# Performance work log

Measured on AMD Instinct MI355X. Metric: run time of the kernel, lower is better.

Reference implementation:

```python
import jax, jax.numpy as jnp
import numpy as np
import math

EMBED_DIMS = 256
NUM_HEADS = 8
NUM_LEVELS = 4
NUM_POINTS = 8
SPATIAL_SHAPES = np.array([[92, 160], [46, 80], [23, 40], [12, 20]], dtype=np.int32)


def _offset_bias():
    # Faithful to reset_parameters(): per-head unit directions scaled by point index.
    thetas = np.arange(NUM_HEADS, dtype=np.float32) * (2.0 * math.pi / NUM_HEADS)
    grid = np.stack([np.cos(thetas), np.sin(thetas)], axis=-1)
    grid = grid / np.abs(grid).max(axis=-1, keepdims=True)
    grid = np.tile(grid[:, None, None, :], (1, NUM_LEVELS, NUM_POINTS, 1))
    for i in range(NUM_POINTS):
        grid[:, :, i, :] *= i + 1
    return grid.reshape(-1).astype(np.float32)


def setup_inputs() -> dict:
    key = jax.random.key(0)
    ks = jax.random.split(key, 8)
    B, Q, E = 4, 10000, EMBED_DIMS
    S = int((SPATIAL_SHAPES[:, 0] * SPATIAL_SHAPES[:, 1]).sum())
    Z = 4  # num_z_anchors; NUM_POINTS % Z == 0
    query = jax.random.normal(ks[0], (B, Q, E), dtype=jnp.float32)
    value = jax.random.normal(ks[1], (B, S, E), dtype=jnp.float32)
    reference_points = jax.random.uniform(ks[2], (B, Q, Z, 2), dtype=jnp.float32)
    # Learned params (random weights so the math is fully exercised; bias per original init).
    w_off = jax.random.normal(ks[3], (E, NUM_HEADS * NUM_LEVELS * NUM_POINTS * 2), dtype=jnp.float32) * 0.01
    b_off = jnp.asarray(_offset_bias())
    w_attn = jax.random.normal(ks[4], (E, NUM_HEADS * NUM_LEVELS * NUM_POINTS), dtype=jnp.float32) * 0.02
    b_attn = jnp.zeros((NUM_HEADS * NUM_LEVELS * NUM_POINTS,), dtype=jnp.float32)
    w_val = jax.random.normal(ks[5], (E, E), dtype=jnp.float32) * (1.0 / np.sqrt(E))
    b_val = jnp.zeros((E,), dtype=jnp.float32)
    return {
        "query": query, "value": value, "reference_points": reference_points,
        "w_off": w_off, "b_off": b_off, "w_attn": w_attn, "b_attn": b_attn,
        "w_val": w_val, "b_val": b_val,
        "spatial_shapes": jnp.asarray(SPATIAL_SHAPES),
    }


def _bilinear_sample(img, px, py):
    """grid_sample(bilinear, padding=zeros, align_corners=False).
    img: [N, H, W, D]; px, py: [N, Q, P] in pixel coords. Returns [N, Q, P, D]."""
    H, W = img.shape[1], img.shape[2]
    x0 = jnp.floor(px); y0 = jnp.floor(py)
    wx = (px - x0)[..., None]; wy = (py - y0)[..., None]
    x0i = x0.astype(jnp.int32); y0i = y0.astype(jnp.int32)
    x1i = x0i + 1; y1i = y0i + 1
    bidx = jnp.arange(img.shape[0])[:, None, None]
    def gather(yy, xx):
        m = ((yy >= 0) & (yy < H) & (xx >= 0) & (xx < W)).astype(img.dtype)[..., None]
        return img[bidx, jnp.clip(yy, 0, H - 1), jnp.clip(xx, 0, W - 1)] * m
    v00 = gather(y0i, x0i); v01 = gather(y0i, x1i)
    v10 = gather(y1i, x0i); v11 = gather(y1i, x1i)
    return (v00 * (1 - wx) + v01 * wx) * (1 - wy) + (v10 * (1 - wx) + v11 * wx) * wy


def _forward(query, value, reference_points, w_off, b_off, w_attn, b_attn, w_val, b_val, shapes_np):
    B, Q, E = query.shape
    NH, L, NP = NUM_HEADS, shapes_np.shape[0], NUM_POINTS
    D = E // NH
    v = (value @ w_val + b_val).reshape(B, -1, NH, D)  # [B, S, NH, D]
    off = (query @ w_off + b_off).reshape(B, Q, NH, L, NP, 2)
    attn = jax.nn.softmax((query @ w_attn + b_attn).reshape(B, Q, NH, L * NP), axis=-1)
    attn = attn.reshape(B, Q, NH, L, NP)
    # Normalize offsets by (W, H) per level.
    norm = jnp.asarray(np.stack([shapes_np[:, 1], shapes_np[:, 0]], axis=-1), dtype=off.dtype)  # [L,2]
    off = off / norm[None, None, None, :, None, :]
    Z = reference_points.shape[2]
    off = off.reshape(B, Q, NH, L, NP // Z, Z, 2)
    loc = reference_points[:, :, None, None, None, :, :] + off  # [B,Q,NH,L,NP/Z,Z,2]
    loc = loc.reshape(B, Q, NH, L, NP, 2)
    out = jnp.zeros((B, Q, NH, D), dtype=query.dtype)
    start = 0
    for lvl in range(L):
        hl, wl = int(shapes_np[lvl, 0]), int(shapes_np[lvl, 1])
        seg = v[:, start:start + hl * wl]
        start += hl * wl
        img = seg.reshape(B, hl, wl, NH, D).transpose(0, 3, 1, 2, 4).reshape(B * NH, hl, wl, D)
        g = loc[:, :, :, lvl].transpose(0, 2, 1, 3, 4).reshape(B * NH, Q, NP, 2)
        # align_corners=False: pixel = norm_coord * size - 0.5
        px = g[..., 0] * wl - 0.5
        py = g[..., 1] * hl - 0.5
        samp = _bilinear_sample(img, px, py)  # [B*NH, Q, NP, D]
        w = attn[:, :, :, lvl].transpose(0, 2, 1, 3).reshape(B * NH, Q, NP)
        out = out + jnp.einsum('nqpd,nqp->nqd', samp, w).reshape(B, NH, Q, D).transpose(0, 2, 1, 3)
    return out.reshape(B, Q, NH * D)


def reference(query, value, reference_points, w_off, b_off, w_attn, b_attn, w_val, b_val, spatial_shapes):
    shapes_np = np.asarray(spatial_shapes)
    return _forward(query, value, reference_points, w_off, b_off, w_attn, b_attn, w_val, b_val, shapes_np)
```

## Files before the change

kernel.cpp:

```cpp
#include <hip/hip_runtime.h>

#define BATCH    4
#define NQ       10000
#define EMB      256
#define NH       8
#define DH       32
#define NL       4
#define NP       8
#define S_TOTAL  19560
#define NROW     (BATCH * NQ)
#define VROWS    (BATCH * S_TOTAL)

typedef _Float16 half8 __attribute__((ext_vector_type(8)));
typedef _Float16 half4v __attribute__((ext_vector_type(4)));
typedef _Float16 half2v __attribute__((ext_vector_type(2)));
typedef float floatx4 __attribute__((ext_vector_type(4)));

__global__ __launch_bounds__(256) void prep_weights(
    const float* __restrict__ w_off, const float* __restrict__ w_attn,
    const float* __restrict__ w_val, _Float16* __restrict__ wT768,
    _Float16* __restrict__ wvaT) {
  const int tid = blockIdx.x * 256 + threadIdx.x;
  const int n = tid >> 8, k = tid & 255;
  const int c = k >> 3, e = k & 7;
  const int swz = ((c ^ (n & 7)) << 3) + e;
  float v;
  _Float16* dst;
  if (n < 512)      { v = w_off[(size_t)k * 512 + n];          dst = wT768 + (size_t)n * 256; }
  else if (n < 768) { v = w_attn[(size_t)k * 256 + (n - 512)]; dst = wT768 + (size_t)n * 256; }
  else              { v = w_val[(size_t)k * 256 + (n - 768)];  dst = wvaT + (size_t)(n - 768) * 256; }
  dst[swz] = (_Float16)v;
}

template <int NC, int NYS, bool SWZ>
__global__ __launch_bounds__(256, 3) void gemm5(
    const float* __restrict__ A, const _Float16* __restrict__ WTs,
    const float* __restrict__ bias0, const float* __restrict__ bias1,
    int splitc, _Float16* __restrict__ C, int M) {
  __shared__ _Float16 bsm[64 * 256];
  const int t = threadIdx.x;
  const int wave = t >> 6, lane = t & 63;
  const int l15 = lane & 15, quad = lane >> 4;
  const int m0 = blockIdx.x * 128 + wave * 32;
  const int nlo = blockIdx.y * (NC / NYS);
  const int nchunks = (NC / NYS) / 64;

  half8 a[2][8];
  #pragma unroll
  for (int i = 0; i < 2; ++i) {
    const float* Ar = A + (size_t)min(m0 + 16 * i + l15, M - 1) * 256 + quad * 8;
    #pragma unroll
    for (int ks = 0; ks < 8; ++ks) {
      const float4 f0 = *(const float4*)(Ar + ks * 32);
      const float4 f1 = *(const float4*)(Ar + ks * 32 + 4);
      a[i][ks][0] = (_Float16)f0.x; a[i][ks][1] = (_Float16)f0.y;
      a[i][ks][2] = (_Float16)f0.z; a[i][ks][3] = (_Float16)f0.w;
      a[i][ks][4] = (_Float16)f1.x; a[i][ks][5] = (_Float16)f1.y;
      a[i][ks][6] = (_Float16)f1.z; a[i][ks][7] = (_Float16)f1.w;
    }
  }

  const _Float16* src = WTs + (size_t)nlo * 256;

  for (int ch = 0; ch < nchunks; ++ch) {
    __syncthreads();
    #pragma unroll
    for (int i = 0; i < 8; ++i)
      *(half8*)&bsm[t * 8 + i * 2048] = *(const half8*)(src + t * 8 + i * 2048);
    __syncthreads();

    floatx4 acc[2][4] = {};
    #pragma unroll
    for (int ks = 0; ks < 8; ++ks) {
      half8 b[4];
      #pragma unroll
      for (int j = 0; j < 4; ++j)
        b[j] = *(const half8*)&bsm[(16 * j + l15) * 256 +
                                   ((((ks * 4 + quad) ^ (l15 & 7))) << 3)];
      #pragma unroll
      for (int j = 0; j < 4; ++j)
        #pragma unroll
        for (int i = 0; i < 2; ++i)
          acc[i][j] = __builtin_amdgcn_mfma_f32_16x16x32_f16(a[i][ks], b[j], acc[i][j], 0, 0, 0);
    }

    const int nc0 = nlo + ch * 64;
    float bc[4];
    #pragma unroll
    for (int j = 0; j < 4; ++j) {
      const int col = nc0 + 16 * j + l15;
      bc[j] = (col < splitc) ? bias0[col] : bias1[col - splitc];
    }

    #pragma unroll
    for (int i = 0; i < 2; ++i) {
      #pragma unroll
      for (int r = 0; r < 4; ++r) {
        const int row = m0 + 16 * i + quad * 4 + r;
        if (row < M) {
          if (SWZ) {
            const int b = row / S_TOTAL;
            const int s = row - b * S_TOTAL;
            #pragma unroll
            for (int j = 0; j < 4; ++j) {
              const int col = nc0 + 16 * j + l15;
              const size_t dst =
                  (((size_t)b * NH + (col >> 5)) * S_TOTAL + s) * 32 + (col & 31);
              C[dst] = (_Float16)(acc[i][j][r] + bc[j]);
            }
          } else {
            #pragma unroll
            for (int j = 0; j < 4; ++j)
              C[(size_t)row * NC + nc0 + 16 * j + l15] =
                  (_Float16)(acc[i][j][r] + bc[j]);
          }
        }
      }
    }
    src += 64 * 256;
  }
}

__global__ __launch_bounds__(256, 4) void msda_sample(
    const _Float16* __restrict__ vproj,
    const _Float16* __restrict__ fused,
    const float* __restrict__ ref,
    float* __restrict__ out) {
  const int lvl_h[NL] = {92, 46, 23, 12};
  const int lvl_w[NL] = {160, 80, 40, 20};
  const int lvl_s[NL] = {0, 14720, 18400, 19320};

  __shared__ int   addr_s[512];
  __shared__ float wl_s[512];
  __shared__ float wr_s[512];

  const int t   = threadIdx.x;
  const int blk = blockIdx.x;
  const int b   = blk & 3;
  const int q   = blk >> 2;
  const int row = b * NQ + q;

  const int h  = t >> 5;
  const int lp = t & 31;
  const int l  = lp >> 3;
  const int p  = lp & 7;

  const float logit = (float)fused[(size_t)row * 768 + 512 + t];
  float mxv = logit;
  #pragma unroll
  for (int m = 1; m < 32; m <<= 1) mxv = fmaxf(mxv, __shfl_xor(mxv, m));
  const float e = __expf(logit - mxv);
  float sum = e;
  #pragma unroll
  for (int m = 1; m < 32; m <<= 1) sum += __shfl_xor(sum, m);
  const float attnw = e / sum;

  const half2v o2 = *(const half2v*)(fused + (size_t)row * 768 + 2 * t);
  const float ox = (float)o2[0], oy = (float)o2[1];
  const int z = p & 3;
  const float rx = ref[((size_t)row * 4 + z) * 2 + 0];
  const float ry = ref[((size_t)row * 4 + z) * 2 + 1];
  const int Wl = lvl_w[l], Hl = lvl_h[l], st = lvl_s[l];

  const float px = fmaf(rx, (float)Wl, ox) - 0.5f;
  const float py = fmaf(ry, (float)Hl, oy) - 0.5f;
  const float x0f = floorf(px), y0f = floorf(py);
  const float wx = px - x0f, wy = py - y0f;
  const int x0 = (int)x0f, y0 = (int)y0f;
  const int x1 = x0 + 1,   y1 = y0 + 1;

  const float mx0 = (x0 >= 0 && x0 < Wl) ? 1.f : 0.f;
  const float mx1 = (x1 >= 0 && x1 < Wl) ? 1.f : 0.f;
  const float my0 = (y0 >= 0 && y0 < Hl) ? 1.f : 0.f;
  const float my1 = (y1 >= 0 && y1 < Hl) ? 1.f : 0.f;
  const int xb  = min(max(x0, -1), Wl - 1);
  const int cy0 = min(max(y0, 0), Hl - 1);
  const int cy1 = min(max(y1, 0), Hl - 1);

  const int bh   = b * NH + h;
  const int lbase = bh * S_TOTAL + st;
  const float wlc = attnw * (1.f - wx) * mx0;
  const float wrc = attnw * wx * mx1;

  addr_s[2 * t + 0] = (lbase + cy0 * Wl + xb) * 32;
  addr_s[2 * t + 1] = (lbase + cy1 * Wl + xb) * 32;
  wl_s[2 * t + 0] = wlc * (1.f - wy) * my0;
  wr_s[2 * t + 0] = wrc * (1.f - wy) * my0;
  wl_s[2 * t + 1] = wlc * wy * my1;
  wr_s[2 * t + 1] = wrc * wy * my1;
  __syncthreads();

  const int g  = t & 31;
  const int c  = g & 7;
  const int sd = (g >> 3) & 1;
  const int ph = g >> 4;
  const int ldoff = sd * 32 + 4 * c;

  half4v vt[16], vb[16];
  float wt[16], wb[16];
  #pragma unroll
  for (int i = 0; i < 16; ++i) {
    const int idx = ((h << 5) + 2 * i + ph) * 2;
    const int at = addr_s[idx], ab = addr_s[idx + 1];
    wt[i] = sd ? wr_s[idx]     : wl_s[idx];
    wb[i] = sd ? wr_s[idx + 1] : wl_s[idx + 1];
    vt[i] = *(const half4v*)(vproj + at + ldoff);
    vb[i] = *(const half4v*)(vproj + ab + ldoff);
  }

  float a0 = 0.f, a1 = 0.f, a2 = 0.f, a3 = 0.f;
  #pragma unroll
  for (int i = 0; i < 16; ++i) {
    a0 = fmaf(wt[i], (float)vt[i][0], a0); a1 = fmaf(wt[i], (float)vt[i][1], a1);
    a2 = fmaf(wt[i], (float)vt[i][2], a2); a3 = fmaf(wt[i], (float)vt[i][3], a3);
    a0 = fmaf(wb[i], (float)vb[i][0], a0); a1 = fmaf(wb[i], (float)vb[i][1], a1);
    a2 = fmaf(wb[i], (float)vb[i][2], a2); a3 = fmaf(wb[i], (float)vb[i][3], a3);
  }

  a0 += __shfl_xor(a0, 8);  a1 += __shfl_xor(a1, 8);
  a2 += __shfl_xor(a2, 8);  a3 += __shfl_xor(a3, 8);
  a0 += __shfl_xor(a0, 16); a1 += __shfl_xor(a1, 16);
  a2 += __shfl_xor(a2, 16); a3 += __shfl_xor(a3, 16);

  if (g < 8) {
    float4 o; o.x = a0; o.y = a1; o.z = a2; o.w = a3;
    *(float4*)(out + (size_t)row * 256 + (h << 5) + 4 * c) = o;
  }
}

extern "C" void kernel_launch(void* const* d_in, const int* in_sizes, int n_in,
                              void* d_out, int out_size, void* d_ws, size_t ws_size,
                              hipStream_t stream) {
  const float* query  = (const float*)d_in[0];
  const float* value  = (const float*)d_in[1];
  const float* refpts = (const float*)d_in[2];
  const float* w_off  = (const float*)d_in[3];
  const float* b_off  = (const float*)d_in[4];
  const float* w_attn = (const float*)d_in[5];
  const float* b_attn = (const float*)d_in[6];
  const float* w_val  = (const float*)d_in[7];
  const float* b_val  = (const float*)d_in[8];
  float* out = (float*)d_out;

  char* p = (char*)d_ws;
  p += 256;
  _Float16* vh    = (_Float16*)p;  p += (size_t)VROWS * 256 * 2;
  p += 256;
  _Float16* wT768 = (_Float16*)p;  p += (size_t)768 * 256 * 2;
  _Float16* wvaT  = (_Float16*)p;  p += (size_t)256 * 256 * 2;
  _Float16* fused_h = (_Float16*)p; p += (size_t)NROW * 768 * 2;

  prep_weights<<<1024, 256, 0, stream>>>(w_off, w_attn, w_val, wT768, wvaT);

  gemm5<256, 1, true><<<dim3((VROWS + 127) / 128, 1), 256, 0, stream>>>(
      value, wvaT, b_val, b_val, 1 << 30, vh, VROWS);
  gemm5<768, 2, false><<<dim3((NROW + 127) / 128, 2), 256, 0, stream>>>(
      query, wT768, b_off, b_attn, 512, fused_h, NROW);

  msda_sample<<<dim3(NROW), 256, 0, stream>>>(vh, fused_h, refpts, out);
}
```

Baseline: 396.9 us.

## Use 512-thread blocks with 16-byte value gathers in deformable sampling

Measured after the change: 434.0 us. 1.09x slower.

```diff
diff --git a/kernel.cpp b/kernel.cpp
--- a/kernel.cpp
+++ b/kernel.cpp
@@ -121,7 +121,7 @@
   }
 }
 
-__global__ __launch_bounds__(256, 4) void msda_sample(
+__global__ __launch_bounds__(512, 6) void msda_sample(
     const _Float16* __restrict__ vproj,
     const _Float16* __restrict__ fused,
     const float* __restrict__ ref,
@@ -131,21 +131,21 @@
   const int lvl_s[NL] = {0, 14720, 18400, 19320};
 
   __shared__ int   addr_s[512];
-  __shared__ float wl_s[512];
-  __shared__ float wr_s[512];
+  __shared__ float w2_s[1024];
 
   const int t   = threadIdx.x;
+  const int t2  = t & 255;
   const int blk = blockIdx.x;
   const int b   = blk & 3;
   const int q   = blk >> 2;
   const int row = b * NQ + q;
 
-  const int h  = t >> 5;
-  const int lp = t & 31;
+  const int h1 = t2 >> 5;
+  const int lp = t2 & 31;
   const int l  = lp >> 3;
   const int p  = lp & 7;
 
-  const float logit = (float)fused[(size_t)row * 768 + 512 + t];
+  const float logit = (float)fused[(size_t)row * 768 + 512 + t2];
   float mxv = logit;
   #pragma unroll
   for (int m = 1; m < 32; m <<= 1) mxv = fmaxf(mxv, __shfl_xor(mxv, m));
@@ -155,7 +155,7 @@
   for (int m = 1; m < 32; m <<= 1) sum += __shfl_xor(sum, m);
   const float attnw = e / sum;
 
-  const half2v o2 = *(const half2v*)(fused + (size_t)row * 768 + 2 * t);
+  const half2v o2 = *(const half2v*)(fused + (size_t)row * 768 + 2 * t2);
   const float ox = (float)o2[0], oy = (float)o2[1];
   const int z = p & 3;
   const float rx = ref[((size_t)row * 4 + z) * 2 + 0];
@@ -177,54 +177,75 @@
   const int cy0 = min(max(y0, 0), Hl - 1);
   const int cy1 = min(max(y1, 0), Hl - 1);
 
-  const int bh   = b * NH + h;
+  const int bh   = b * NH + h1;
   const int lbase = bh * S_TOTAL + st;
   const float wlc = attnw * (1.f - wx) * mx0;
   const float wrc = attnw * wx * mx1;
 
-  addr_s[2 * t + 0] = (lbase + cy0 * Wl + xb) * 32;
-  addr_s[2 * t + 1] = (lbase + cy1 * Wl + xb) * 32;
-  wl_s[2 * t + 0] = wlc * (1.f - wy) * my0;
-  wr_s[2 * t + 0] = wrc * (1.f - wy) * my0;
-  wl_s[2 * t + 1] = wlc * wy * my1;
-  wr_s[2 * t + 1] = wrc * wy * my1;
+  addr_s[2 * t2 + 0] = (lbase + cy0 * Wl + xb) * 32;
+  addr_s[2 * t2 + 1] = (lbase + cy1 * Wl + xb) * 32;
+  w2_s[2 * t2 + 0]       = wlc * (1.f - wy) * my0;
+  w2_s[2 * t2 + 1]       = wlc * wy * my1;
+  w2_s[512 + 2 * t2 + 0] = wrc * (1.f - wy) * my0;
+  w2_s[512 + 2 * t2 + 1] = wrc * wy * my1;
   __syncthreads();
 
-  const int g  = t & 31;
-  const int c  = g & 7;
-  const int sd = (g >> 3) & 1;
-  const int ph = g >> 4;
-  const int ldoff = sd * 32 + 4 * c;
-
-  half4v vt[16], vb[16];
-  float wt[16], wb[16];
-  #pragma unroll
-  for (int i = 0; i < 16; ++i) {
-    const int idx = ((h << 5) + 2 * i + ph) * 2;
-    const int at = addr_s[idx], ab = addr_s[idx + 1];
-    wt[i] = sd ? wr_s[idx]     : wl_s[idx];
-    wb[i] = sd ? wr_s[idx + 1] : wl_s[idx + 1];
-    vt[i] = *(const half4v*)(vproj + at + ldoff);
-    vb[i] = *(const half4v*)(vproj + ab + ldoff);
-  }
-
-  float a0 = 0.f, a1 = 0.f, a2 = 0.f, a3 = 0.f;
-  #pragma unroll
-  for (int i = 0; i < 16; ++i) {
-    a0 = fmaf(wt[i], (float)vt[i][0], a0); a1 = fmaf(wt[i], (float)vt[i][1], a1);
-    a2 = fmaf(wt[i], (float)vt[i][2], a2); a3 = fmaf(wt[i], (float)vt[i][3], a3);
-    a0 = fmaf(wb[i], (float)vb[i][0], a0); a1 = fmaf(wb[i], (float)vb[i][1], a1);
-    a2 = fmaf(wb[i], (float)vb[i][2], a2); a3 = fmaf(wb[i], (float)vb[i][3], a3);
-  }
-
-  a0 += __shfl_xor(a0, 8);  a1 += __shfl_xor(a1, 8);
-  a2 += __shfl_xor(a2, 8);  a3 += __shfl_xor(a3, 8);
-  a0 += __shfl_xor(a0, 16); a1 += __shfl_xor(a1, 16);
-  a2 += __shfl_xor(a2, 16); a3 += __shfl_xor(a3, 16);
-
-  if (g < 8) {
-    float4 o; o.x = a0; o.y = a1; o.z = a2; o.w = a3;
-    *(float4*)(out + (size_t)row * 256 + (h << 5) + 4 * c) = o;
+  const int h  = t >> 6;
+  const int g  = t & 63;
+  const int c2 = g & 3;
+  const int sd = (g >> 2) & 1;
+  const int pp = g >> 3;
+  const int ldoff = sd * 32 + 8 * c2;
+  const int wbase = sd << 9;
+
+  int bidx[4];
+  #pragma unroll
+  for (int ii = 0; ii < 4; ++ii)
+    bidx[ii] = ((h << 5) + (ii << 3) + pp) << 1;
+
+  int at[4], ab[4];
+  #pragma unroll
+  for (int ii = 0; ii < 4; ++ii) {
+    at[ii] = addr_s[bidx[ii]];
+    ab[ii] = addr_s[bidx[ii] + 1];
+  }
+
+  half8 vt[4], vb[4];
+  #pragma unroll
+  for (int ii = 0; ii < 4; ++ii) {
+    vt[ii] = *(const half8*)(vproj + at[ii] + ldoff);
+    vb[ii] = *(const half8*)(vproj + ab[ii] + ldoff);
+  }
+
+  float wt[4], wb[4];
+  #pragma unroll
+  for (int ii = 0; ii < 4; ++ii) {
+    wt[ii] = w2_s[wbase + bidx[ii]];
+    wb[ii] = w2_s[wbase + bidx[ii] + 1];
+  }
+
+  float a[8] = {0.f, 0.f, 0.f, 0.f, 0.f, 0.f, 0.f, 0.f};
+  #pragma unroll
+  for (int ii = 0; ii < 4; ++ii) {
+    #pragma unroll
+    for (int ch = 0; ch < 8; ++ch) {
+      a[ch] = fmaf(wt[ii], (float)vt[ii][ch], a[ch]);
+      a[ch] = fmaf(wb[ii], (float)vb[ii][ch], a[ch]);
+    }
+  }
+
+  #pragma unroll
+  for (int m = 4; m <= 32; m <<= 1) {
+    #pragma unroll
+    for (int ch = 0; ch < 8; ++ch) a[ch] += __shfl_xor(a[ch], m);
+  }
+
+  if ((g & 60) == 0) {
+    float* op = out + (size_t)row * 256 + (h << 5) + (c2 << 3);
+    float4 o0; o0.x = a[0]; o0.y = a[1]; o0.z = a[2]; o0.w = a[3];
+    float4 o1; o1.x = a[4]; o1.y = a[5]; o1.z = a[6]; o1.w = a[7];
+    *(float4*)op = o0;
+    *(float4*)(op + 4) = o1;
   }
 }
 
@@ -257,5 +278,5 @@
   gemm5<768, 2, false><<<dim3((NROW + 127) / 128, 2), 256, 0, stream>>>(
       query, wT768, b_off, b_attn, 512, fused_h, NROW);
 
-  msda_sample<<<dim3(NROW), 256, 0, stream>>>(vh, fused_h, refpts, out);
-}
+  msda_sample<<<dim3(NROW), 512, 0, stream>>>(vh, fused_h, refpts, out);
+}
```

## Prefetch weight chunks in GEMM, transpose MFMA for packed stores, merge sampler weights

Applied to the files above, without the earlier changes.

Result: no change. 398.2 us (+0.3%).

```diff
diff --git a/kernel.cpp b/kernel.cpp
--- a/kernel.cpp
+++ b/kernel.cpp
@@ -33,7 +33,7 @@
 }
 
 template <int NC, int NYS, bool SWZ>
-__global__ __launch_bounds__(256, 3) void gemm5(
+__global__ __launch_bounds__(256, 3) void gemm6(
     const float* __restrict__ A, const _Float16* __restrict__ WTs,
     const float* __restrict__ bias0, const float* __restrict__ bias1,
     int splitc, _Float16* __restrict__ C, int M) {
@@ -45,6 +45,13 @@
   const int nlo = blockIdx.y * (NC / NYS);
   const int nchunks = (NC / NYS) / 64;
 
+  const _Float16* src = WTs + (size_t)nlo * 256;
+
+  half8 pb[8];
+  #pragma unroll
+  for (int i = 0; i < 8; ++i)
+    pb[i] = *(const half8*)(src + t * 8 + i * 2048);
+
   half8 a[2][8];
   #pragma unroll
   for (int i = 0; i < 2; ++i) {
@@ -60,14 +67,18 @@
     }
   }
 
-  const _Float16* src = WTs + (size_t)nlo * 256;
+  #pragma unroll
+  for (int i = 0; i < 8; ++i)
+    *(half8*)&bsm[t * 8 + i * 2048] = pb[i];
+  __syncthreads();
 
   for (int ch = 0; ch < nchunks; ++ch) {
-    __syncthreads();
-    #pragma unroll
-    for (int i = 0; i < 8; ++i)
-      *(half8*)&bsm[t * 8 + i * 2048] = *(const half8*)(src + t * 8 + i * 2048);
-    __syncthreads();
+    if (ch + 1 < nchunks) {
+      const _Float16* s2 = src + (size_t)(ch + 1) * 64 * 256;
+      #pragma unroll
+      for (int i = 0; i < 8; ++i)
+        pb[i] = *(const half8*)(s2 + t * 8 + i * 2048);
+    }
 
     floatx4 acc[2][4] = {};
     #pragma unroll
@@ -77,38 +88,57 @@
       for (int j = 0; j < 4; ++j)
         b[j] = *(const half8*)&bsm[(16 * j + l15) * 256 +
                                    ((((ks * 4 + quad) ^ (l15 & 7))) << 3)];
-      #pragma unroll
-      for (int j = 0; j < 4; ++j)
-        #pragma unroll
-        for (int i = 0; i < 2; ++i)
-          acc[i][j] = __builtin_amdgcn_mfma_f32_16x16x32_f16(a[i][ks], b[j], acc[i][j], 0, 0, 0);
+      if constexpr (SWZ) {
+        #pragma unroll
+        for (int j = 0; j < 4; ++j)
+          #pragma unroll
+          for (int i = 0; i < 2; ++i)
+            acc[i][j] = __builtin_amdgcn_mfma_f32_16x16x32_f16(b[j], a[i][ks], acc[i][j], 0, 0, 0);
+      } else {
+        #pragma unroll
+        for (int j = 0; j < 4; ++j)
+          #pragma unroll
+          for (int i = 0; i < 2; ++i)
+            acc[i][j] = __builtin_amdgcn_mfma_f32_16x16x32_f16(a[i][ks], b[j], acc[i][j], 0, 0, 0);
+      }
     }
 
     const int nc0 = nlo + ch * 64;
-    float bc[4];
-    #pragma unroll
-    for (int j = 0; j < 4; ++j) {
-      const int col = nc0 + 16 * j + l15;
-      bc[j] = (col < splitc) ? bias0[col] : bias1[col - splitc];
-    }
-
-    #pragma unroll
-    for (int i = 0; i < 2; ++i) {
-      #pragma unroll
-      for (int r = 0; r < 4; ++r) {
-        const int row = m0 + 16 * i + quad * 4 + r;
-        if (row < M) {
-          if (SWZ) {
+
+    if constexpr (SWZ) {
+      #pragma unroll
+      for (int j = 0; j < 4; ++j) {
+        const int col0 = nc0 + 16 * j + quad * 4;
+        const int h = col0 >> 5, c0 = col0 & 31;
+        const float4 bq = *(const float4*)(bias0 + col0);
+        #pragma unroll
+        for (int i = 0; i < 2; ++i) {
+          const int row = m0 + 16 * i + l15;
+          if (row < M) {
             const int b = row / S_TOTAL;
             const int s = row - b * S_TOTAL;
-            #pragma unroll
-            for (int j = 0; j < 4; ++j) {
-              const int col = nc0 + 16 * j + l15;
-              const size_t dst =
-                  (((size_t)b * NH + (col >> 5)) * S_TOTAL + s) * 32 + (col & 31);
-              C[dst] = (_Float16)(acc[i][j][r] + bc[j]);
-            }
-          } else {
+            half4v pk;
+            pk[0] = (_Float16)(acc[i][j][0] + bq.x);
+            pk[1] = (_Float16)(acc[i][j][1] + bq.y);
+            pk[2] = (_Float16)(acc[i][j][2] + bq.z);
+            pk[3] = (_Float16)(acc[i][j][3] + bq.w);
+            *(half4v*)(C + ((((size_t)b * NH + h) * S_TOTAL + s) * 32 + c0)) = pk;
+          }
+        }
+      }
+    } else {
+      float bc[4];
+      #pragma unroll
+      for (int j = 0; j < 4; ++j) {
+        const int col = nc0 + 16 * j + l15;
+        bc[j] = (col < splitc) ? bias0[col] : bias1[col - splitc];
+      }
+      #pragma unroll
+      for (int i = 0; i < 2; ++i) {
+        #pragma unroll
+        for (int r = 0; r < 4; ++r) {
+          const int row = m0 + 16 * i + quad * 4 + r;
+          if (row < M) {
             #pragma unroll
             for (int j = 0; j < 4; ++j)
               C[(size_t)row * NC + nc0 + 16 * j + l15] =
@@ -117,7 +147,14 @@
         }
       }
     }
-    src += 64 * 256;
+
+    __syncthreads();
+    if (ch + 1 < nchunks) {
+      #pragma unroll
+      for (int i = 0; i < 8; ++i)
+        *(half8*)&bsm[t * 8 + i * 2048] = pb[i];
+      __syncthreads();
+    }
   }
 }
 
@@ -131,8 +168,7 @@
   const int lvl_s[NL] = {0, 14720, 18400, 19320};
 
   __shared__ int   addr_s[512];
-  __shared__ float wl_s[512];
-  __shared__ float wr_s[512];
+  __shared__ float w2_s[1024];
 
   const int t   = threadIdx.x;
   const int blk = blockIdx.x;
@@ -184,10 +220,10 @@
 
   addr_s[2 * t + 0] = (lbase + cy0 * Wl + xb) * 32;
   addr_s[2 * t + 1] = (lbase + cy1 * Wl + xb) * 32;
-  wl_s[2 * t + 0] = wlc * (1.f - wy) * my0;
-  wr_s[2 * t + 0] = wrc * (1.f - wy) * my0;
-  wl_s[2 * t + 1] = wlc * wy * my1;
-  wr_s[2 * t + 1] = wrc * wy * my1;
+  w2_s[2 * t + 0]       = wlc * (1.f - wy) * my0;
+  w2_s[2 * t + 1]       = wlc * wy * my1;
+  w2_s[512 + 2 * t + 0] = wrc * (1.f - wy) * my0;
+  w2_s[512 + 2 * t + 1] = wrc * wy * my1;
   __syncthreads();
 
   const int g  = t & 31;
@@ -195,6 +231,7 @@
   const int sd = (g >> 3) & 1;
   const int ph = g >> 4;
   const int ldoff = sd * 32 + 4 * c;
+  const int wbase = sd << 9;
 
   half4v vt[16], vb[16];
   float wt[16], wb[16];
@@ -202,8 +239,8 @@
   for (int i = 0; i < 16; ++i) {
     const int idx = ((h << 5) + 2 * i + ph) * 2;
     const int at = addr_s[idx], ab = addr_s[idx + 1];
-    wt[i] = sd ? wr_s[idx]     : wl_s[idx];
-    wb[i] = sd ? wr_s[idx + 1] : wl_s[idx + 1];
+    wt[i] = w2_s[wbase + idx];
+    wb[i] = w2_s[wbase + idx + 1];
     vt[i] = *(const half4v*)(vproj + at + ldoff);
     vb[i] = *(const half4v*)(vproj + ab + ldoff);
   }
@@ -252,9 +289,9 @@
 
   prep_weights<<<1024, 256, 0, stream>>>(w_off, w_attn, w_val, wT768, wvaT);
 
-  gemm5<256, 1, true><<<dim3((VROWS + 127) / 128, 1), 256, 0, stream>>>(
+  gemm6<256, 1, true><<<dim3((VROWS + 127) / 128, 1), 256, 0, stream>>>(
       value, wvaT, b_val, b_val, 1 << 30, vh, VROWS);
-  gemm5<768, 2, false><<<dim3((NROW + 127) / 128, 2), 256, 0, stream>>>(
+  gemm6<768, 2, false><<<dim3((NROW + 127) / 128, 2), 256, 0, stream>>>(
       query, wT768, b_off, b_attn, 512, fused_h, NROW);
 
   msda_sample<<<dim3(NROW), 256, 0, stream>>>(vh, fused_h, refpts, out);
```
